# Kernel tuning notes

Hardware: AMD Instinct MI355X
Metric: run time of the kernel (lower is better)

## Reference

```python
import jax, jax.numpy as jnp
import numpy as np

H, FH, D = 8, 4, 64          # num_heads, focal_heads, att_size
HID = H * D                   # hidden_size = 512
B, S = 8, 512                 # batch, num_nodes
T_HOP, T_EDGE = 32, 16
SCALE = D ** -0.5


def setup_inputs() -> dict:
    key = jax.random.key(0)
    ks = jax.random.split(key, 24)
    f = lambda i, shape: jax.random.normal(ks[i], shape, jnp.float32)
    w = 1.0 / np.sqrt(HID)
    inp = {
        'q': f(0, (B, S, HID)), 'k': f(1, (B, S, HID)), 'v': f(2, (B, S, HID)),
        'query_hop_emb': f(3, (T_HOP, HID)) * 0.02,
        'query_edge_emb': f(4, (T_EDGE, HID)) * 0.02,
        'key_hop_emb': f(5, (T_HOP, HID)) * 0.02,
        'key_edge_emb': f(6, (T_EDGE, HID)) * 0.02,
        'value_hop_emb': f(7, (T_HOP, HID)) * 0.02,
        'value_edge_emb': f(8, (T_EDGE, HID)) * 0.02,
        'distance': jax.random.randint(ks[9], (B, S, S), 0, T_HOP),
        'edge_attr': jax.random.randint(ks[10], (B, S, S), 0, T_EDGE),
        # guarantee at least one unmasked key per query row to keep softmax finite
        'mask': jax.random.bernoulli(ks[11], 0.9, (B, S)).at[:, 0].set(True),
        'focal_mask': jax.random.bernoulli(ks[12], 0.5, (B, S, S)).at[:, :, 0].set(True),
        'Wq': f(13, (HID, H * D)) * w, 'bq': f(14, (H * D,)) * 0.01,
        'Wk': f(15, (HID, H * D)) * w, 'bk': f(16, (H * D,)) * 0.01,
        'Wv': f(17, (HID, H * D)) * w, 'bv': f(18, (H * D,)) * 0.01,
        'Wo': f(19, (H * D, HID)) * w, 'bo': f(20, (HID,)) * 0.01,
    }
    return inp


def _emb_scores(x, emb):
    # x: [B,H,S,D], emb: [T, H*D] -> per-head scores [B,H,S,T]
    e = emb.reshape(-1, H, D).transpose(1, 0, 2)  # [H,T,D]
    return jnp.einsum('bhsd,htd->bhst', x, e)


def _gather_last(scores, idx):
    # scores: [B,H,S,T], idx: [B,S,S] -> [B,H,S,S]
    idx_b = jnp.broadcast_to(idx[:, None], (B, H, S, S))
    return jnp.take_along_axis(scores, idx_b, axis=3)


def _scatter_add_last(attn, idx, T):
    # attn: [B,H,S,S], idx: [B,S,S] -> [B,H,S,T] accumulating attn weights
    idx_b = jnp.broadcast_to(idx[:, None], (B, H, S, S)).reshape(B * H * S, S)
    rows = jnp.arange(B * H * S)[:, None]
    flat = (rows * T + idx_b).reshape(-1)
    out = jnp.zeros((B * H * S * T,), attn.dtype).at[flat].add(attn.reshape(-1))
    return out.reshape(B, H, S, T)


def reference(q, k, v, query_hop_emb, query_edge_emb, key_hop_emb, key_edge_emb,
              value_hop_emb, value_edge_emb, distance, edge_attr, mask, focal_mask,
              Wq, bq, Wk, bk, Wv, bv, Wo, bo):
    qh = (q @ Wq + bq).reshape(B, S, H, D).transpose(0, 2, 1, 3)  # [B,H,S,D]
    kh = (k @ Wk + bk).reshape(B, S, H, D).transpose(0, 2, 1, 3)
    vh = (v @ Wv + bv).reshape(B, S, H, D).transpose(0, 2, 1, 3)

    spatial_bias = (_gather_last(_emb_scores(qh, query_hop_emb), distance)
                    + _gather_last(_emb_scores(kh, key_hop_emb), distance))
    edge_bias = (_gather_last(_emb_scores(qh, query_edge_emb), edge_attr)
                 + _gather_last(_emb_scores(kh, key_edge_emb), edge_attr))

    attn = (jnp.einsum('bhsd,bhtd->bhst', qh, kh) + spatial_bias + edge_bias) * SCALE

    GS = H - FH
    a1 = jnp.where(mask[:, None, None, :], attn[:, :GS], -jnp.inf)
    a2 = jnp.where(focal_mask[:, None], attn[:, GS:], -jnp.inf)
    attn = jax.nn.softmax(jnp.concatenate([a1, a2], axis=1), axis=3)

    vha = _scatter_add_last(attn, distance, T_HOP)   # [B,H,S,T_HOP]
    vea = _scatter_add_last(attn, edge_attr, T_EDGE)  # [B,H,S,T_EDGE]
    vh_emb = value_hop_emb.reshape(T_HOP, H, D).transpose(1, 0, 2)   # [H,T,D]
    ve_emb = value_edge_emb.reshape(T_EDGE, H, D).transpose(1, 0, 2)

    x = (jnp.einsum('bhst,bhtd->bhsd', attn, vh)
         + jnp.einsum('bhst,htd->bhsd', vha, vh_emb)
         + jnp.einsum('bhst,htd->bhsd', vea, ve_emb))
    x = x.transpose(0, 2, 1, 3).reshape(B, S, H * D)
    return x @ Wo + bo
```

## Files before the change

### kernel.cpp

```cpp
#include <hip/hip_runtime.h>

constexpr int nB = 8, nS = 512, nH = 8, nD = 64, nHID = 512;
constexpr int THOP = 32, TEDGE = 16;
constexpr float SCALE = 0.125f;
constexpr float NEGINF = -30000.0f;

typedef __attribute__((ext_vector_type(8))) short bf16x8;
typedef __attribute__((ext_vector_type(4))) float f32x4;

#define MFMA16(A, B, C) __builtin_amdgcn_mfma_f32_16x16x32_bf16(A, B, C, 0, 0, 0)

__device__ __align__(16) unsigned short g_qhi[(size_t)nB * nH * nS * nD];
__device__ __align__(16) unsigned short g_qlo[(size_t)nB * nH * nS * nD];
__device__ __align__(16) unsigned short g_khi[(size_t)nB * nH * nS * nD];
__device__ __align__(16) unsigned short g_klo[(size_t)nB * nH * nS * nD];
__device__ __align__(16) unsigned short g_vhiT[(size_t)nB * nH * nD * nS];
__device__ __align__(16) unsigned short g_vloT[(size_t)nB * nH * nD * nS];
__device__ __align__(16) unsigned short g_embh[96 * 512];
__device__ __align__(16) unsigned short g_embl[96 * 512];
__device__ __align__(16) unsigned short g_inhi[(size_t)3 * 2097152];
__device__ __align__(16) unsigned short g_inlo[(size_t)3 * 2097152];
__device__ __align__(16) unsigned short g_wth[(size_t)4 * 262144];
__device__ __align__(16) unsigned short g_wtl[(size_t)4 * 262144];
__device__ __align__(16) unsigned short g_xhi[(size_t)nB * nS * nHID];
__device__ __align__(16) unsigned short g_xlo[(size_t)nB * nS * nHID];
__device__ int g_flags[32];

__device__ __forceinline__ float ldf(const void* p, int isf32, size_t i) {
  if (isf32) return ((const float*)p)[i];
  unsigned int w = (unsigned int)(((const unsigned short*)p)[i]) << 16;
  return __uint_as_float(w);
}
__device__ __forceinline__ float bf2f(unsigned short h) {
  return __uint_as_float((unsigned)h << 16);
}
__device__ __forceinline__ float4 ldf4(const void* p, int isf32, size_t i) {
  if (isf32) return ((const float4*)p)[i >> 2];
  const ushort4 u = ((const ushort4*)p)[i >> 2];
  float4 r;
  r.x = bf2f(u.x); r.y = bf2f(u.y); r.z = bf2f(u.z); r.w = bf2f(u.w);
  return r;
}
__device__ __forceinline__ unsigned short f2bf(float x) {
  unsigned u = __float_as_uint(x);
  u += 0x7FFFu + ((u >> 16) & 1u);
  return (unsigned short)(u >> 16);
}

__device__ int detect_bool_mode(const unsigned char* p) {
  if (p[0] == 0x80 && p[1] == 0x3F) return 2;
  if (p[0] == 0x00 && p[1] == 0x3C) return 4;
  if (p[0] == 0x00 && p[3] == 0x3F) return 3;
  for (int i = 0; i < 64; i += 4)
    if (p[i + 1] | p[i + 2] | p[i + 3]) return 1;
  return 0;
}
__device__ __forceinline__ bool bool_at(const unsigned char* p, int mode, size_t i) {
  switch (mode) {
    case 0: return ((const int*)p)[i] != 0;
    case 1: return p[i] != 0;
    case 3: return ((const float*)p)[i] != 0.f;
    default: return ((const unsigned short*)p)[i] != 0;
  }
}

__global__ __launch_bounds__(256) void detect_all(
    const void* q, const void* k, const void* v,
    const void* qhe, const void* qee, const void* khe, const void* kee,
    const void* vhe, const void* vee,
    const int* dist, const int* edge,
    const unsigned char* mraw, const unsigned char* fraw,
    const void* Wq, const void* bq, const void* Wk, const void* bk,
    const void* Wv, const void* bv, const void* Wo, const void* bo) {
  __shared__ float sred[256];
  __shared__ int nzs;
  const int tid = threadIdx.x;
  const int blk = blockIdx.x;

  if (blk < 17) {
    const void* arrs[17] = {q, k, v, qhe, qee, khe, kee, vhe, vee,
                            Wq, bq, Wk, bk, Wv, bv, Wo, bo};
    const int full[17] = {2097152, 2097152, 2097152, 8192, 8192, 8192, 8192,
                          8192, 8192, 262144, 512, 262144, 512, 262144, 512,
                          262144, 512};
    const int n = full[blk] < 16384 ? full[blk] : 16384;
    const unsigned short* u = (const unsigned short*)arrs[blk];
    float m = 0.f;
    for (int i = tid; i < n; i += 256) {
      float x = __uint_as_float((unsigned int)u[i] << 16);
      if (x != x) x = 1e20f;
      m = fmaxf(m, fabsf(x));
    }
    sred[tid] = m;
    __syncthreads();
    for (int s = 128; s > 0; s >>= 1) {
      if (tid < s) sred[tid] = fmaxf(sred[tid], sred[tid + s]);
      __syncthreads();
    }
    if (tid == 0) g_flags[4 + blk] = (sred[0] > 1e3f) ? 1 : 0;
  } else if (blk == 17 || blk == 18) {
    const int* p = (blk == 17) ? dist : edge;
    if (tid == 0) nzs = 0;
    __syncthreads();
    int a = 0;
    for (int i = tid; i < 4096; i += 256) a |= p[2 * i + 1];
    if (a) atomicOr(&nzs, 1);
    __syncthreads();
    if (tid == 0) g_flags[blk - 17] = (nzs == 0);
  } else {
    if (tid == 0) {
      g_flags[2] = detect_bool_mode(mraw);
      g_flags[3] = detect_bool_mode(fraw);
    }
  }
}

__global__ __launch_bounds__(256) void emb_prep(
    const void* qhe, const void* khe, const void* qee, const void* kee) {
  const int blk = blockIdx.x;
  const void* srcs[4] = {qhe, khe, qee, kee};
  const int flagIdx[4] = {7, 9, 8, 10};
  const int counts[4] = {32 * 512, 32 * 512, 16 * 512, 16 * 512};
  const int dsts[4] = {0, 32 * 512, 64 * 512, 80 * 512};
  const int f = g_flags[flagIdx[blk]];
  const void* src = srcs[blk];
  const int n = counts[blk], d0 = dsts[blk];
  for (int i = threadIdx.x; i < n; i += 256) {
    const float x = ldf(src, f, i);
    const unsigned short hi = f2bf(x);
    g_embh[d0 + i] = hi;
    g_embl[d0 + i] = f2bf(x - bf2f(hi));
  }
}

__global__ __launch_bounds__(256) void split_prep(
    const void* q, const void* k, const void* v) {
  const int t = blockIdx.y;
  const void* srcs[3] = {q, k, v};
  const int f = g_flags[4 + t];
  const size_t base = (size_t)t * 2097152;
  const size_t i = ((size_t)blockIdx.x * 256 + threadIdx.x) * 4;
  const float4 v4 = ldf4(srcs[t], f, i);
  ushort4 h4, l4;
  h4.x = f2bf(v4.x); l4.x = f2bf(v4.x - bf2f(h4.x));
  h4.y = f2bf(v4.y); l4.y = f2bf(v4.y - bf2f(h4.y));
  h4.z = f2bf(v4.z); l4.z = f2bf(v4.z - bf2f(h4.z));
  h4.w = f2bf(v4.w); l4.w = f2bf(v4.w - bf2f(h4.w));
  *(ushort4*)&g_inhi[base + i] = h4;
  *(ushort4*)&g_inlo[base + i] = l4;
}

__global__ __launch_bounds__(256) void wt_prep(
    const void* Wq, const void* Wk, const void* Wv, const void* Wo) {
  __shared__ float t[64][65];
  const int mat = blockIdx.y;
  const void* srcs[4] = {Wq, Wk, Wv, Wo};
  const int fIdx[4] = {13, 15, 17, 19};
  const int f = g_flags[fIdx[mat]];
  const void* W = srcs[mat];
  const int k0 = (blockIdx.x >> 3) * 64, n0 = (blockIdx.x & 7) * 64;
  const int tid = threadIdx.x;
  const int r = tid >> 4, c4 = (tid & 15) * 4;
#pragma unroll
  for (int i = 0; i < 4; ++i) {
    const float4 v4 = ldf4(W, f, (size_t)(k0 + r + i * 16) * 512 + n0 + c4);
    t[r + i * 16][c4] = v4.x;
    t[r + i * 16][c4 + 1] = v4.y;
    t[r + i * 16][c4 + 2] = v4.z;
    t[r + i * 16][c4 + 3] = v4.w;
  }
  __syncthreads();
  unsigned short* dh = g_wth + (size_t)mat * 262144;
  unsigned short* dl = g_wtl + (size_t)mat * 262144;
#pragma unroll
  for (int i = 0; i < 4; ++i) {
    const int rn = r + i * 16;
    ushort4 h4, l4;
    const float v0 = t[c4][rn], v1 = t[c4 + 1][rn];
    const float v2 = t[c4 + 2][rn], v3 = t[c4 + 3][rn];
    h4.x = f2bf(v0); l4.x = f2bf(v0 - bf2f(h4.x));
    h4.y = f2bf(v1); l4.y = f2bf(v1 - bf2f(h4.y));
    h4.z = f2bf(v2); l4.z = f2bf(v2 - bf2f(h4.z));
    h4.w = f2bf(v3); l4.w = f2bf(v3 - bf2f(h4.w));
    *(ushort4*)&dh[(size_t)(n0 + rn) * 512 + k0 + c4] = h4;
    *(ushort4*)&dl[(size_t)(n0 + rn) * 512 + k0 + c4] = l4;
  }
}

__global__ __launch_bounds__(256) void gemm_mfma(
    const unsigned short* __restrict__ Ahi, const unsigned short* __restrict__ Alo,
    const unsigned short* __restrict__ Wth, const unsigned short* __restrict__ Wtl,
    const void* __restrict__ bias, int bFlag,
    float* __restrict__ dst, int mode) {
  __shared__ unsigned short As_hi[64][40];
  __shared__ unsigned short As_lo[64][40];
  __shared__ unsigned short Wt_hi[64][40];
  __shared__ unsigned short Wt_lo[64][40];
  const int bF = g_flags[bFlag];
  const int tid = threadIdx.x;
  const int m0 = blockIdx.y * 64, n0 = blockIdx.x * 64;
  const int w = tid >> 6, l = tid & 63, c = l & 15, g = l >> 4;
  const int wr = w >> 1, wc = w & 1;
  const int sr = tid >> 2, sc = (tid & 3) * 8;

  f32x4 acc[2][2] = {{{0.f, 0.f, 0.f, 0.f}, {0.f, 0.f, 0.f, 0.f}},
                     {{0.f, 0.f, 0.f, 0.f}, {0.f, 0.f, 0.f, 0.f}}};

  for (int k0 = 0; k0 < 512; k0 += 32) {
    __syncthreads();
    {
      const size_t ga = (size_t)(m0 + sr) * 512 + k0 + sc;
      const size_t gw = (size_t)(n0 + sr) * 512 + k0 + sc;
      const bf16x8 ah = *(const bf16x8*)(Ahi + ga);
      const bf16x8 al = *(const bf16x8*)(Alo + ga);
      const bf16x8 wh = *(const bf16x8*)(Wth + gw);
      const bf16x8 wl = *(const bf16x8*)(Wtl + gw);
      *(bf16x8*)&As_hi[sr][sc] = ah;
      *(bf16x8*)&As_lo[sr][sc] = al;
      *(bf16x8*)&Wt_hi[sr][sc] = wh;
      *(bf16x8*)&Wt_lo[sr][sc] = wl;
    }
    __syncthreads();
#pragma unroll
    for (int mi = 0; mi < 2; ++mi) {
      const bf16x8 ah = *(const bf16x8*)&As_hi[wr * 32 + mi * 16 + c][g * 8];
      const bf16x8 al = *(const bf16x8*)&As_lo[wr * 32 + mi * 16 + c][g * 8];
#pragma unroll
      for (int nj = 0; nj < 2; ++nj) {
        const bf16x8 wh = *(const bf16x8*)&Wt_hi[wc * 32 + nj * 16 + c][g * 8];
        const bf16x8 wl = *(const bf16x8*)&Wt_lo[wc * 32 + nj * 16 + c][g * 8];
        acc[mi][nj] = MFMA16(ah, wh, acc[mi][nj]);
        acc[mi][nj] = MFMA16(al, wh, acc[mi][nj]);
        acc[mi][nj] = MFMA16(ah, wl, acc[mi][nj]);
      }
    }
  }
#pragma unroll
  for (int mi = 0; mi < 2; ++mi)
#pragma unroll
    for (int nj = 0; nj < 2; ++nj)
#pragma unroll
      for (int r = 0; r < 4; ++r) {
        const int m = m0 + wr * 32 + mi * 16 + 4 * g + r;
        const int n = n0 + wc * 32 + nj * 16 + c;
        const float v2 = acc[mi][nj][r] + ldf(bias, bF, n);
        if (mode == 3) {
          dst[(size_t)m * 512 + n] = v2;
        } else {
          const int b = m >> 9, s = m & 511, h = n >> 6, d = n & 63;
          const unsigned short hi = f2bf(v2);
          const unsigned short lo = f2bf(v2 - bf2f(hi));
          if (mode == 0) {
            const size_t i0 = (((size_t)(b * nH + h) * nS) + s) * nD + d;
            g_qhi[i0] = hi; g_qlo[i0] = lo;
          } else if (mode == 1) {
            const size_t i0 = (((size_t)(b * nH + h) * nS) + s) * nD + d;
            g_khi[i0] = hi; g_klo[i0] = lo;
          } else {
            const size_t i0 = (((size_t)(b * nH + h) * nD) + d) * nS + s;
            g_vhiT[i0] = hi; g_vloT[i0] = lo;
          }
        }
      }
}

__global__ __launch_bounds__(256) void attn_kernel(
    const int* __restrict__ dist, const int* __restrict__ edge,
    const unsigned char* __restrict__ mraw, const unsigned char* __restrict__ fraw,
    const void* __restrict__ vhe, const void* __restrict__ vee) {
  __shared__ float chop_s[16][33];
  __shared__ float cedge_s[16][17];
  __shared__ float vha_s[16][33];
  __shared__ float vea_s[16][17];
  __shared__ float red_s[16][4];
  __shared__ float red2_s[16][4];
  __shared__ float rinv_s[16];
  __shared__ float x_s[64][17];
  __shared__ unsigned char dlds[16][516];
  __shared__ unsigned char elds[16][516];
  __shared__ unsigned char flds[16][516];
  __shared__ unsigned char smask_l[516];

  const int bh = blockIdx.x, qt = blockIdx.y;
  const int b = bh >> 3, h = bh & 7;
  const int q0 = qt * 16;
  const int tid = threadIdx.x;
  const int w = tid >> 6, l = tid & 63, c = l & 15, g = l >> 4;

  const int d64 = g_flags[0], e64 = g_flags[1];
  const int mmode = g_flags[2], fmode = g_flags[3];
  const int fvhe = g_flags[11], fvee = g_flags[12];

  for (int i = tid; i < 16 * 33; i += 256) (&vha_s[0][0])[i] = 0.f;
  for (int i = tid; i < 16 * 17; i += 256) (&vea_s[0][0])[i] = 0.f;
  for (int i = tid; i < 64 * 17; i += 256) (&x_s[0][0])[i] = 0.f;

  const size_t rowbase = ((size_t)b * nS + q0) * nS;
  if (!d64) {
    const int4* dp = (const int4*)(dist + rowbase);
    for (int j4 = tid; j4 < 2048; j4 += 256) {
      const int4 t = dp[j4];
      const int j = j4 * 4, r = j >> 9, c1 = j & 511;
      *(unsigned*)&dlds[r][c1] =
          (unsigned)(t.x & 31) | ((unsigned)(t.y & 31) << 8) |
          ((unsigned)(t.z & 31) << 16) | ((unsigned)(t.w & 31) << 24);
    }
  } else {
    const int4* dp = (const int4*)(dist + 2 * rowbase);
    for (int j2 = tid; j2 < 4096; j2 += 256) {
      const int4 t = dp[j2];
      const int j = j2 * 2, r = j >> 9, c1 = j & 511;
      *(unsigned short*)&dlds[r][c1] =
          (unsigned short)((t.x & 31) | ((t.z & 31) << 8));
    }
  }
  if (!e64) {
    const int4* ep = (const int4*)(edge + rowbase);
    for (int j4 = tid; j4 < 2048; j4 += 256) {
      const int4 t = ep[j4];
      const int j = j4 * 4, r = j >> 9, c1 = j & 511;
      *(unsigned*)&elds[r][c1] =
          (unsigned)(t.x & 15) | ((unsigned)(t.y & 15) << 8) |
          ((unsigned)(t.z & 15) << 16) | ((unsigned)(t.w & 15) << 24);
    }
  } else {
    const int4* ep = (const int4*)(edge + 2 * rowbase);
    for (int j2 = tid; j2 < 4096; j2 += 256) {
      const int4 t = ep[j2];
      const int j = j2 * 2, r = j >> 9, c1 = j & 511;
      *(unsigned short*)&elds[r][c1] =
          (unsigned short)((t.x & 15) | ((t.z & 15) << 8));
    }
  }
  if (h < 4) {
    for (int i4 = tid; i4 < 128; i4 += 256) {
      unsigned wv = 0;
#pragma unroll
      for (int t = 0; t < 4; ++t)
        wv |= (unsigned)bool_at(mraw, mmode, (size_t)b * nS + i4 * 4 + t) << (8 * t);
      *(unsigned*)&smask_l[i4 * 4] = wv;
    }
  } else {
    for (int i4 = tid; i4 < 2048; i4 += 256) {
      const int j = i4 * 4, r = j >> 9, c1 = j & 511;
      unsigned wv = 0;
#pragma unroll
      for (int t = 0; t < 4; ++t)
        wv |= (unsigned)bool_at(fraw, fmode, rowbase + j + t) << (8 * t);
      *(unsigned*)&flds[r][c1] = wv;
    }
  }

  const size_t qbase = (((size_t)bh * nS) + q0 + c) * nD + g * 8;
  const bf16x8 qh0 = *(const bf16x8*)(g_qhi + qbase);
  const bf16x8 qh1 = *(const bf16x8*)(g_qhi + qbase + 32);
  const bf16x8 ql0 = *(const bf16x8*)(g_qlo + qbase);
  const bf16x8 ql1 = *(const bf16x8*)(g_qlo + qbase + 32);

  if (w < 3) {
    const bool isEdge = (w == 2);
    const int tb = (w == 1) ? 16 : 0;
    const size_t qe0 = (isEdge ? (size_t)64 * 512 : 0) + (size_t)(tb + c) * 512 + h * 64;
    const size_t ke0 = (isEdge ? (size_t)80 * 512 : (size_t)32 * 512) + (size_t)(tb + c) * 512 + h * 64;
    f32x4 acc = {0.f, 0.f, 0.f, 0.f};
#pragma unroll
    for (int dh = 0; dh < 2; ++dh) {
      const bf16x8 qhh = dh ? qh1 : qh0;
      const bf16x8 qll = dh ? ql1 : ql0;
      const bf16x8 khq = *(const bf16x8*)(g_khi + qbase + dh * 32);
      const bf16x8 klq = *(const bf16x8*)(g_klo + qbase + dh * 32);
      const bf16x8 eqh = *(const bf16x8*)(g_embh + qe0 + dh * 32 + g * 8);
      const bf16x8 eql = *(const bf16x8*)(g_embl + qe0 + dh * 32 + g * 8);
      const bf16x8 ekh = *(const bf16x8*)(g_embh + ke0 + dh * 32 + g * 8);
      const bf16x8 ekl = *(const bf16x8*)(g_embl + ke0 + dh * 32 + g * 8);
      acc = MFMA16(qhh, eqh, acc);
      acc = MFMA16(qll, eqh, acc);
      acc = MFMA16(qhh, eql, acc);
      acc = MFMA16(khq, ekh, acc);
      acc = MFMA16(klq, ekh, acc);
      acc = MFMA16(khq, ekl, acc);
    }
    if (!isEdge) {
#pragma unroll
      for (int r = 0; r < 4; ++r) chop_s[4 * g + r][tb + c] = acc[r];
    } else {
#pragma unroll
      for (int r = 0; r < 4; ++r) cedge_s[4 * g + r][c] = acc[r];
    }
  }
  __syncthreads();

  f32x4 pS[8];
  const int kbw = w * 128;
#pragma unroll
  for (int kt = 0; kt < 8; ++kt) {
    const int kb = kbw + kt * 16;
    const size_t kbase = (((size_t)bh * nS) + kb + c) * nD + g * 8;
    f32x4 acc = {0.f, 0.f, 0.f, 0.f};
    {
      const bf16x8 kh0 = *(const bf16x8*)(g_khi + kbase);
      const bf16x8 kl0 = *(const bf16x8*)(g_klo + kbase);
      acc = MFMA16(kh0, qh0, acc);
      acc = MFMA16(kl0, qh0, acc);
      acc = MFMA16(kh0, ql0, acc);
      const bf16x8 kh1 = *(const bf16x8*)(g_khi + kbase + 32);
      const bf16x8 kl1 = *(const bf16x8*)(g_klo + kbase + 32);
      acc = MFMA16(kh1, qh1, acc);
      acc = MFMA16(kl1, qh1, acc);
      acc = MFMA16(kh1, ql1, acc);
    }
    const int key0 = kb + 4 * g;
    const unsigned dw = *(const unsigned*)&dlds[c][key0];
    const unsigned ew = *(const unsigned*)&elds[c][key0];
    const unsigned fw = (h < 4) ? *(const unsigned*)&smask_l[key0]
                                : *(const unsigned*)&flds[c][key0];
#pragma unroll
    for (int r = 0; r < 4; ++r) {
      const int dv = (dw >> (8 * r)) & 255;
      const int ev = (ew >> (8 * r)) & 255;
      const float s = (acc[r] + chop_s[c][dv] + cedge_s[c][ev]) * SCALE;
      pS[kt][r] = ((fw >> (8 * r)) & 255) ? s : NEGINF;
    }
  }

  float mx = NEGINF;
#pragma unroll
  for (int kt = 0; kt < 8; ++kt)
#pragma unroll
    for (int r = 0; r < 4; ++r) mx = fmaxf(mx, pS[kt][r]);
  mx = fmaxf(mx, __shfl_xor(mx, 16));
  mx = fmaxf(mx, __shfl_xor(mx, 32));
  if (l < 16) red_s[c][w] = mx;
  __syncthreads();
  const float M = fmaxf(fmaxf(red_s[c][0], red_s[c][1]),
                        fmaxf(red_s[c][2], red_s[c][3]));
  float sum = 0.f;
#pragma unroll
  for (int kt = 0; kt < 8; ++kt) {
    const int key0 = kbw + kt * 16 + 4 * g;
    const unsigned dw = *(const unsigned*)&dlds[c][key0];
    const unsigned ew = *(const unsigned*)&elds[c][key0];
#pragma unroll
    for (int r = 0; r < 4; ++r) {
      const float pv = __expf(pS[kt][r] - M);
      pS[kt][r] = pv;
      sum += pv;
      atomicAdd(&vha_s[c][(dw >> (8 * r)) & 255], pv);
      atomicAdd(&vea_s[c][(ew >> (8 * r)) & 255], pv);
    }
  }
  sum += __shfl_xor(sum, 16);
  sum += __shfl_xor(sum, 32);
  if (l < 16) red2_s[c][w] = sum;
  int pk[8][2];
#pragma unroll
  for (int kt = 0; kt < 8; ++kt) {
    pk[kt][0] = ((int)f2bf(pS[kt][1]) << 16) | (int)f2bf(pS[kt][0]);
    pk[kt][1] = ((int)f2bf(pS[kt][3]) << 16) | (int)f2bf(pS[kt][2]);
  }
  __syncthreads();
  if (w == 0 && l < 16) {
    const float tot = red2_s[c][0] + red2_s[c][1] + red2_s[c][2] + red2_s[c][3];
    rinv_s[c] = 1.0f / tot;
  }

  f32x4 oacc[4] = {{0.f, 0.f, 0.f, 0.f}, {0.f, 0.f, 0.f, 0.f},
                   {0.f, 0.f, 0.f, 0.f}, {0.f, 0.f, 0.f, 0.f}};
  const int srcA = ((g & 1) * 2) * 16 + c;
  const int srcB = srcA + 16;
  const bool hi2 = (g >> 1) != 0;
#pragma unroll
  for (int ks = 0; ks < 4; ++ks) {
    const int t0d0 = __shfl(pk[2 * ks][0], srcA);
    const int t1d0 = __shfl(pk[2 * ks + 1][0], srcA);
    const int t0d1 = __shfl(pk[2 * ks][1], srcA);
    const int t1d1 = __shfl(pk[2 * ks + 1][1], srcA);
    const int t0d0b = __shfl(pk[2 * ks][0], srcB);
    const int t1d0b = __shfl(pk[2 * ks + 1][0], srcB);
    const int t0d1b = __shfl(pk[2 * ks][1], srcB);
    const int t1d1b = __shfl(pk[2 * ks + 1][1], srcB);
    union { int i[4]; bf16x8 v; } bu;
    bu.i[0] = hi2 ? t1d0 : t0d0;
    bu.i[1] = hi2 ? t1d1 : t0d1;
    bu.i[2] = hi2 ? t1d0b : t0d0b;
    bu.i[3] = hi2 ? t1d1b : t0d1b;
    const int kk = w * 128 + ks * 32;
#pragma unroll
    for (int t = 0; t < 4; ++t) {
      const size_t vbase = (((size_t)bh * nD) + t * 16 + c) * nS + kk + g * 8;
      const bf16x8 vh_ = *(const bf16x8*)(g_vhiT + vbase);
      const bf16x8 vl_ = *(const bf16x8*)(g_vloT + vbase);
      oacc[t] = MFMA16(vh_, bu.v, oacc[t]);
      oacc[t] = MFMA16(vl_, bu.v, oacc[t]);
    }
  }
#pragma unroll
  for (int t = 0; t < 4; ++t)
#pragma unroll
    for (int r = 0; r < 4; ++r)
      atomicAdd(&x_s[t * 16 + 4 * g + r][c], oacc[t][r]);
  __syncthreads();

  {
    const int d = tid & 63, qq = tid >> 6;
    float val[4];
#pragma unroll
    for (int j = 0; j < 4; ++j) val[j] = x_s[d][qq + 4 * j];
    for (int t = 0; t < THOP; ++t) {
      const float e = ldf(vhe, fvhe, (size_t)t * nHID + h * 64 + d);
#pragma unroll
      for (int j = 0; j < 4; ++j) val[j] += vha_s[qq + 4 * j][t] * e;
    }
    for (int t = 0; t < TEDGE; ++t) {
      const float e = ldf(vee, fvee, (size_t)t * nHID + h * 64 + d);
#pragma unroll
      for (int j = 0; j < 4; ++j) val[j] += vea_s[qq + 4 * j][t] * e;
    }
#pragma unroll
    for (int j = 0; j < 4; ++j) {
      const int q = qq + 4 * j;
      const float xv = val[j] * rinv_s[q];
      const unsigned short hi = f2bf(xv);
      const size_t i0 = ((size_t)b * nS + q0 + q) * nHID + h * 64 + d;
      g_xhi[i0] = hi;
      g_xlo[i0] = f2bf(xv - bf2f(hi));
    }
  }
}

extern "C" void kernel_launch(void* const* d_in, const int* in_sizes, int n_in,
                              void* d_out, int out_size, void* d_ws, size_t ws_size,
                              hipStream_t stream) {
  const void* q   = d_in[0];
  const void* k   = d_in[1];
  const void* v   = d_in[2];
  const void* qhe = d_in[3];
  const void* qee = d_in[4];
  const void* khe = d_in[5];
  const void* kee = d_in[6];
  const void* vhe = d_in[7];
  const void* vee = d_in[8];
  const int* dist = (const int*)d_in[9];
  const int* edge = (const int*)d_in[10];
  const unsigned char* mraw = (const unsigned char*)d_in[11];
  const unsigned char* fraw = (const unsigned char*)d_in[12];
  const void* Wq = d_in[13];
  const void* bq = d_in[14];
  const void* Wk = d_in[15];
  const void* bk = d_in[16];
  const void* Wv = d_in[17];
  const void* bv = d_in[18];
  const void* Wo = d_in[19];
  const void* bo = d_in[20];

  detect_all<<<20, 256, 0, stream>>>(q, k, v, qhe, qee, khe, kee, vhe, vee,
                                     dist, edge, mraw, fraw,
                                     Wq, bq, Wk, bk, Wv, bv, Wo, bo);
  emb_prep<<<4, 256, 0, stream>>>(qhe, khe, qee, kee);
  split_prep<<<dim3(2048, 3), 256, 0, stream>>>(q, k, v);
  wt_prep<<<dim3(64, 4), 256, 0, stream>>>(Wq, Wk, Wv, Wo);

  unsigned short* inhi; hipGetSymbolAddress((void**)&inhi, HIP_SYMBOL(g_inhi));
  unsigned short* inlo; hipGetSymbolAddress((void**)&inlo, HIP_SYMBOL(g_inlo));
  unsigned short* wth;  hipGetSymbolAddress((void**)&wth,  HIP_SYMBOL(g_wth));
  unsigned short* wtl;  hipGetSymbolAddress((void**)&wtl,  HIP_SYMBOL(g_wtl));
  unsigned short* xhi;  hipGetSymbolAddress((void**)&xhi,  HIP_SYMBOL(g_xhi));
  unsigned short* xlo;  hipGetSymbolAddress((void**)&xlo,  HIP_SYMBOL(g_xlo));

  gemm_mfma<<<dim3(8, 64), 256, 0, stream>>>(inhi, inlo, wth, wtl,
                                             bq, 14, nullptr, 0);
  gemm_mfma<<<dim3(8, 64), 256, 0, stream>>>(inhi + 2097152, inlo + 2097152,
                                             wth + 262144, wtl + 262144,
                                             bk, 16, nullptr, 1);
  gemm_mfma<<<dim3(8, 64), 256, 0, stream>>>(inhi + 2 * 2097152, inlo + 2 * 2097152,
                                             wth + 2 * 262144, wtl + 2 * 262144,
                                             bv, 18, nullptr, 2);
  attn_kernel<<<dim3(64, 32), 256, 0, stream>>>(dist, edge, mraw, fraw, vhe, vee);
  gemm_mfma<<<dim3(8, 64), 256, 0, stream>>>(xhi, xlo,
                                             wth + 3 * 262144, wtl + 3 * 262144,
                                             bo, 20, (float*)d_out, 3);
}
```

Before: 661.8 us.

## Stage K/V tiles in swizzled LDS, pack indices/masks, prefetch GEMM tiles, remap blocks

The projection GEMM now prefetches the next k-slice into registers while computing on the current LDS tile, a form of software pipelining. The attention kernel packs distance, edge and mask into one 16-bit word per key in shared memory. It stages K in 64-row chunks and V-hi in 128-column chunks into XOR-swizzled shared buffers, cooperatively loaded, instead of per-lane global loads. Blocks are remapped so consecutive block IDs span different batch-heads, and x_s reuses the packed-index buffer to cut LDS footprint. The cost is many extra __syncthreads in the key and value loops and larger LDS use, which may lower occupancy.

```diff
diff --git a/kernel.cpp b/kernel.cpp
--- a/kernel.cpp
+++ b/kernel.cpp
@@ -206,21 +206,26 @@
   f32x4 acc[2][2] = {{{0.f, 0.f, 0.f, 0.f}, {0.f, 0.f, 0.f, 0.f}},
                      {{0.f, 0.f, 0.f, 0.f}, {0.f, 0.f, 0.f, 0.f}}};
 
+  const size_t ga = (size_t)(m0 + sr) * 512 + sc;
+  const size_t gw = (size_t)(n0 + sr) * 512 + sc;
+  bf16x8 pa_h = *(const bf16x8*)(Ahi + ga);
+  bf16x8 pa_l = *(const bf16x8*)(Alo + ga);
+  bf16x8 pw_h = *(const bf16x8*)(Wth + gw);
+  bf16x8 pw_l = *(const bf16x8*)(Wtl + gw);
+
   for (int k0 = 0; k0 < 512; k0 += 32) {
     __syncthreads();
-    {
-      const size_t ga = (size_t)(m0 + sr) * 512 + k0 + sc;
-      const size_t gw = (size_t)(n0 + sr) * 512 + k0 + sc;
-      const bf16x8 ah = *(const bf16x8*)(Ahi + ga);
-      const bf16x8 al = *(const bf16x8*)(Alo + ga);
-      const bf16x8 wh = *(const bf16x8*)(Wth + gw);
-      const bf16x8 wl = *(const bf16x8*)(Wtl + gw);
-      *(bf16x8*)&As_hi[sr][sc] = ah;
-      *(bf16x8*)&As_lo[sr][sc] = al;
-      *(bf16x8*)&Wt_hi[sr][sc] = wh;
-      *(bf16x8*)&Wt_lo[sr][sc] = wl;
-    }
-    __syncthreads();
+    *(bf16x8*)&As_hi[sr][sc] = pa_h;
+    *(bf16x8*)&As_lo[sr][sc] = pa_l;
+    *(bf16x8*)&Wt_hi[sr][sc] = pw_h;
+    *(bf16x8*)&Wt_lo[sr][sc] = pw_l;
+    __syncthreads();
+    if (k0 < 480) {
+      pa_h = *(const bf16x8*)(Ahi + ga + k0 + 32);
+      pa_l = *(const bf16x8*)(Alo + ga + k0 + 32);
+      pw_h = *(const bf16x8*)(Wth + gw + k0 + 32);
+      pw_l = *(const bf16x8*)(Wtl + gw + k0 + 32);
+    }
 #pragma unroll
     for (int mi = 0; mi < 2; ++mi) {
       const bf16x8 ah = *(const bf16x8*)&As_hi[wr * 32 + mi * 16 + c][g * 8];
@@ -268,6 +273,8 @@
     const int* __restrict__ dist, const int* __restrict__ edge,
     const unsigned char* __restrict__ mraw, const unsigned char* __restrict__ fraw,
     const void* __restrict__ vhe, const void* __restrict__ vee) {
+  __shared__ unsigned short kvbuf[8192];
+  __shared__ unsigned short plds[16][520];
   __shared__ float chop_s[16][33];
   __shared__ float cedge_s[16][17];
   __shared__ float vha_s[16][33];
@@ -275,13 +282,10 @@
   __shared__ float red_s[16][4];
   __shared__ float red2_s[16][4];
   __shared__ float rinv_s[16];
-  __shared__ float x_s[64][17];
-  __shared__ unsigned char dlds[16][516];
-  __shared__ unsigned char elds[16][516];
-  __shared__ unsigned char flds[16][516];
-  __shared__ unsigned char smask_l[516];
-
-  const int bh = blockIdx.x, qt = blockIdx.y;
+
+  const int id = blockIdx.x;
+  const int bh = (id & 7) * 8 + ((id >> 3) & 7);
+  const int qt = id >> 6;
   const int b = bh >> 3, h = bh & 7;
   const int q0 = qt * 16;
   const int tid = threadIdx.x;
@@ -293,62 +297,36 @@
 
   for (int i = tid; i < 16 * 33; i += 256) (&vha_s[0][0])[i] = 0.f;
   for (int i = tid; i < 16 * 17; i += 256) (&vea_s[0][0])[i] = 0.f;
-  for (int i = tid; i < 64 * 17; i += 256) (&x_s[0][0])[i] = 0.f;
 
   const size_t rowbase = ((size_t)b * nS + q0) * nS;
-  if (!d64) {
-    const int4* dp = (const int4*)(dist + rowbase);
-    for (int j4 = tid; j4 < 2048; j4 += 256) {
-      const int4 t = dp[j4];
-      const int j = j4 * 4, r = j >> 9, c1 = j & 511;
-      *(unsigned*)&dlds[r][c1] =
-          (unsigned)(t.x & 31) | ((unsigned)(t.y & 31) << 8) |
-          ((unsigned)(t.z & 31) << 16) | ((unsigned)(t.w & 31) << 24);
-    }
-  } else {
-    const int4* dp = (const int4*)(dist + 2 * rowbase);
-    for (int j2 = tid; j2 < 4096; j2 += 256) {
-      const int4 t = dp[j2];
-      const int j = j2 * 2, r = j >> 9, c1 = j & 511;
-      *(unsigned short*)&dlds[r][c1] =
-          (unsigned short)((t.x & 31) | ((t.z & 31) << 8));
-    }
-  }
-  if (!e64) {
-    const int4* ep = (const int4*)(edge + rowbase);
-    for (int j4 = tid; j4 < 2048; j4 += 256) {
-      const int4 t = ep[j4];
-      const int j = j4 * 4, r = j >> 9, c1 = j & 511;
-      *(unsigned*)&elds[r][c1] =
-          (unsigned)(t.x & 15) | ((unsigned)(t.y & 15) << 8) |
-          ((unsigned)(t.z & 15) << 16) | ((unsigned)(t.w & 15) << 24);
-    }
-  } else {
-    const int4* ep = (const int4*)(edge + 2 * rowbase);
-    for (int j2 = tid; j2 < 4096; j2 += 256) {
-      const int4 t = ep[j2];
-      const int j = j2 * 2, r = j >> 9, c1 = j & 511;
-      *(unsigned short*)&elds[r][c1] =
-          (unsigned short)((t.x & 15) | ((t.z & 15) << 8));
-    }
-  }
-  if (h < 4) {
-    for (int i4 = tid; i4 < 128; i4 += 256) {
-      unsigned wv = 0;
-#pragma unroll
-      for (int t = 0; t < 4; ++t)
-        wv |= (unsigned)bool_at(mraw, mmode, (size_t)b * nS + i4 * 4 + t) << (8 * t);
-      *(unsigned*)&smask_l[i4 * 4] = wv;
-    }
-  } else {
-    for (int i4 = tid; i4 < 2048; i4 += 256) {
-      const int j = i4 * 4, r = j >> 9, c1 = j & 511;
-      unsigned wv = 0;
-#pragma unroll
-      for (int t = 0; t < 4; ++t)
-        wv |= (unsigned)bool_at(fraw, fmode, rowbase + j + t) << (8 * t);
-      *(unsigned*)&flds[r][c1] = wv;
-    }
+  for (int j4 = tid; j4 < 2048; j4 += 256) {
+    const int j = j4 * 4, r = j >> 9, c1 = j & 511;
+    int dv[4], ev[4];
+    if (!d64) {
+      const int4 t = ((const int4*)(dist + rowbase))[j4];
+      dv[0] = t.x & 31; dv[1] = t.y & 31; dv[2] = t.z & 31; dv[3] = t.w & 31;
+    } else {
+      const int4 t0 = ((const int4*)(dist + 2 * rowbase))[2 * j4];
+      const int4 t1 = ((const int4*)(dist + 2 * rowbase))[2 * j4 + 1];
+      dv[0] = t0.x & 31; dv[1] = t0.z & 31; dv[2] = t1.x & 31; dv[3] = t1.z & 31;
+    }
+    if (!e64) {
+      const int4 t = ((const int4*)(edge + rowbase))[j4];
+      ev[0] = t.x & 15; ev[1] = t.y & 15; ev[2] = t.z & 15; ev[3] = t.w & 15;
+    } else {
+      const int4 t0 = ((const int4*)(edge + 2 * rowbase))[2 * j4];
+      const int4 t1 = ((const int4*)(edge + 2 * rowbase))[2 * j4 + 1];
+      ev[0] = t0.x & 15; ev[1] = t0.z & 15; ev[2] = t1.x & 15; ev[3] = t1.z & 15;
+    }
+    ushort4 pw;
+    unsigned short* pp = (unsigned short*)&pw;
+#pragma unroll
+    for (int t = 0; t < 4; ++t) {
+      const bool keep = (h < 4) ? bool_at(mraw, mmode, (size_t)b * nS + c1 + t)
+                                : bool_at(fraw, fmode, rowbase + j + t);
+      pp[t] = (unsigned short)(dv[t] | (ev[t] << 5) | ((int)keep << 9));
+    }
+    *(ushort4*)&plds[r][c1] = pw;
   }
 
   const size_t qbase = (((size_t)bh * nS) + q0 + c) * nD + g * 8;
@@ -388,38 +366,59 @@
       for (int r = 0; r < 4; ++r) cedge_s[4 * g + r][c] = acc[r];
     }
   }
+
+#pragma unroll
+  for (int it = 0; it < 2; ++it) {
+    const int e = (tid << 3) + (it << 11);
+    const int r = e >> 6, d0 = e & 63;
+    const size_t src = (((size_t)bh * nS) + r) * nD + d0;
+    const int dsti = (r << 6) + ((((d0 >> 3) ^ (r & 7))) << 3);
+    *(bf16x8*)&kvbuf[dsti] = *(const bf16x8*)(g_khi + src);
+    *(bf16x8*)&kvbuf[4096 + dsti] = *(const bf16x8*)(g_klo + src);
+  }
   __syncthreads();
 
   f32x4 pS[8];
-  const int kbw = w * 128;
-#pragma unroll
-  for (int kt = 0; kt < 8; ++kt) {
-    const int kb = kbw + kt * 16;
-    const size_t kbase = (((size_t)bh * nS) + kb + c) * nD + g * 8;
+  const int sw8 = c & 7;
+  for (int ch = 0; ch < 8; ++ch) {
+    const int rloc = w * 16 + c;
+    const int a0 = rloc << 6;
     f32x4 acc = {0.f, 0.f, 0.f, 0.f};
     {
-      const bf16x8 kh0 = *(const bf16x8*)(g_khi + kbase);
-      const bf16x8 kl0 = *(const bf16x8*)(g_klo + kbase);
+      const int o0 = a0 + ((g ^ sw8) << 3);
+      const int o1 = a0 + ((((4 + g) ^ sw8)) << 3);
+      const bf16x8 kh0 = *(const bf16x8*)&kvbuf[o0];
+      const bf16x8 kl0 = *(const bf16x8*)&kvbuf[4096 + o0];
+      const bf16x8 kh1 = *(const bf16x8*)&kvbuf[o1];
+      const bf16x8 kl1 = *(const bf16x8*)&kvbuf[4096 + o1];
       acc = MFMA16(kh0, qh0, acc);
       acc = MFMA16(kl0, qh0, acc);
       acc = MFMA16(kh0, ql0, acc);
-      const bf16x8 kh1 = *(const bf16x8*)(g_khi + kbase + 32);
-      const bf16x8 kl1 = *(const bf16x8*)(g_klo + kbase + 32);
       acc = MFMA16(kh1, qh1, acc);
       acc = MFMA16(kl1, qh1, acc);
       acc = MFMA16(kh1, ql1, acc);
     }
-    const int key0 = kb + 4 * g;
-    const unsigned dw = *(const unsigned*)&dlds[c][key0];
-    const unsigned ew = *(const unsigned*)&elds[c][key0];
-    const unsigned fw = (h < 4) ? *(const unsigned*)&smask_l[key0]
-                                : *(const unsigned*)&flds[c][key0];
+    const int key0 = ch * 64 + w * 16 + 4 * g;
+    const ushort4 pv4 = *(const ushort4*)&plds[c][key0];
+    const unsigned short pp[4] = {pv4.x, pv4.y, pv4.z, pv4.w};
 #pragma unroll
     for (int r = 0; r < 4; ++r) {
-      const int dv = (dw >> (8 * r)) & 255;
-      const int ev = (ew >> (8 * r)) & 255;
-      const float s = (acc[r] + chop_s[c][dv] + cedge_s[c][ev]) * SCALE;
-      pS[kt][r] = ((fw >> (8 * r)) & 255) ? s : NEGINF;
+      const float s = (acc[r] + chop_s[c][pp[r] & 31] +
+                       cedge_s[c][(pp[r] >> 5) & 15]) * SCALE;
+      pS[ch][r] = (pp[r] & 512) ? s : NEGINF;
+    }
+    __syncthreads();
+    if (ch < 7) {
+#pragma unroll
+      for (int it = 0; it < 2; ++it) {
+        const int e = (tid << 3) + (it << 11);
+        const int r = e >> 6, d0 = e & 63;
+        const size_t src = (((size_t)bh * nS) + (ch + 1) * 64 + r) * nD + d0;
+        const int dsti = (r << 6) + ((((d0 >> 3) ^ (r & 7))) << 3);
+        *(bf16x8*)&kvbuf[dsti] = *(const bf16x8*)(g_khi + src);
+        *(bf16x8*)&kvbuf[4096 + dsti] = *(const bf16x8*)(g_klo + src);
+      }
+      __syncthreads();
     }
   }
 
@@ -437,16 +436,16 @@
   float sum = 0.f;
 #pragma unroll
   for (int kt = 0; kt < 8; ++kt) {
-    const int key0 = kbw + kt * 16 + 4 * g;
-    const unsigned dw = *(const unsigned*)&dlds[c][key0];
-    const unsigned ew = *(const unsigned*)&elds[c][key0];
+    const int key0 = kt * 64 + w * 16 + 4 * g;
+    const ushort4 pv4 = *(const ushort4*)&plds[c][key0];
+    const unsigned short pp[4] = {pv4.x, pv4.y, pv4.z, pv4.w};
 #pragma unroll
     for (int r = 0; r < 4; ++r) {
       const float pv = __expf(pS[kt][r] - M);
       pS[kt][r] = pv;
       sum += pv;
-      atomicAdd(&vha_s[c][(dw >> (8 * r)) & 255], pv);
-      atomicAdd(&vea_s[c][(ew >> (8 * r)) & 255], pv);
+      atomicAdd(&vha_s[c][pp[r] & 31], pv);
+      atomicAdd(&vea_s[c][(pp[r] >> 5) & 15], pv);
     }
   }
   sum += __shfl_xor(sum, 16);
@@ -459,40 +458,53 @@
     pk[kt][1] = ((int)f2bf(pS[kt][3]) << 16) | (int)f2bf(pS[kt][2]);
   }
   __syncthreads();
+  float (*x_s)[17] = reinterpret_cast<float(*)[17]>(&plds[0][0]);
+  for (int i = tid; i < 64 * 17; i += 256) (&x_s[0][0])[i] = 0.f;
   if (w == 0 && l < 16) {
     const float tot = red2_s[c][0] + red2_s[c][1] + red2_s[c][2] + red2_s[c][3];
     rinv_s[c] = 1.0f / tot;
   }
+  __syncthreads();
 
   f32x4 oacc[4] = {{0.f, 0.f, 0.f, 0.f}, {0.f, 0.f, 0.f, 0.f},
                    {0.f, 0.f, 0.f, 0.f}, {0.f, 0.f, 0.f, 0.f}};
   const int srcA = ((g & 1) * 2) * 16 + c;
   const int srcB = srcA + 16;
   const bool hi2 = (g >> 1) != 0;
-#pragma unroll
-  for (int ks = 0; ks < 4; ++ks) {
-    const int t0d0 = __shfl(pk[2 * ks][0], srcA);
-    const int t1d0 = __shfl(pk[2 * ks + 1][0], srcA);
-    const int t0d1 = __shfl(pk[2 * ks][1], srcA);
-    const int t1d1 = __shfl(pk[2 * ks + 1][1], srcA);
-    const int t0d0b = __shfl(pk[2 * ks][0], srcB);
-    const int t1d0b = __shfl(pk[2 * ks + 1][0], srcB);
-    const int t0d1b = __shfl(pk[2 * ks][1], srcB);
-    const int t1d1b = __shfl(pk[2 * ks + 1][1], srcB);
+  for (int p = 0; p < 4; ++p) {
+#pragma unroll
+    for (int it = 0; it < 4; ++it) {
+      const int e = (tid << 3) + (it << 11);
+      const int d = e >> 7, colc = e & 127;
+      const size_t src = (((size_t)bh * nD) + d) * nS + (p << 7) + colc;
+      const int dsti = (d << 7) + ((((colc >> 3) ^ (d & 15))) << 3);
+      *(bf16x8*)&kvbuf[dsti] = *(const bf16x8*)(g_vhiT + src);
+    }
+    __syncthreads();
+    const int t0d0 = __shfl(pk[2 * p][0], srcA);
+    const int t1d0 = __shfl(pk[2 * p + 1][0], srcA);
+    const int t0d1 = __shfl(pk[2 * p][1], srcA);
+    const int t1d1 = __shfl(pk[2 * p + 1][1], srcA);
+    const int t0d0b = __shfl(pk[2 * p][0], srcB);
+    const int t1d0b = __shfl(pk[2 * p + 1][0], srcB);
+    const int t0d1b = __shfl(pk[2 * p][1], srcB);
+    const int t1d1b = __shfl(pk[2 * p + 1][1], srcB);
     union { int i[4]; bf16x8 v; } bu;
     bu.i[0] = hi2 ? t1d0 : t0d0;
     bu.i[1] = hi2 ? t1d1 : t0d1;
     bu.i[2] = hi2 ? t1d0b : t0d0b;
     bu.i[3] = hi2 ? t1d1b : t0d1b;
-    const int kk = w * 128 + ks * 32;
+    const int col16 = (w << 1) + (g & 1) + ((g >> 1) << 3);
+    const int j0 = (p << 7) + ((g >> 1) << 6) + (w << 4) + ((g & 1) << 3);
 #pragma unroll
     for (int t = 0; t < 4; ++t) {
-      const size_t vbase = (((size_t)bh * nD) + t * 16 + c) * nS + kk + g * 8;
-      const bf16x8 vh_ = *(const bf16x8*)(g_vhiT + vbase);
-      const bf16x8 vl_ = *(const bf16x8*)(g_vloT + vbase);
+      const int row = t * 16 + c;
+      const bf16x8 vh_ = *(const bf16x8*)&kvbuf[(row << 7) + (((col16 ^ c)) << 3)];
+      const bf16x8 vl_ = *(const bf16x8*)(g_vloT + (((size_t)bh * nD) + row) * nS + j0);
       oacc[t] = MFMA16(vh_, bu.v, oacc[t]);
       oacc[t] = MFMA16(vl_, bu.v, oacc[t]);
     }
+    __syncthreads();
   }
 #pragma unroll
   for (int t = 0; t < 4; ++t)
@@ -575,7 +587,7 @@
   gemm_mfma<<<dim3(8, 64), 256, 0, stream>>>(inhi + 2 * 2097152, inlo + 2 * 2097152,
                                              wth + 2 * 262144, wtl + 2 * 262144,
                                              bv, 18, nullptr, 2);
-  attn_kernel<<<dim3(64, 32), 256, 0, stream>>>(dist, edge, mraw, fraw, vhe, vee);
+  attn_kernel<<<2048, 256, 0, stream>>>(dist, edge, mraw, fraw, vhe, vee);
   gemm_mfma<<<dim3(8, 64), 256, 0, stream>>>(xhi, xlo,
                                              wth + 3 * 262144, wtl + 3 * 262144,
                                              bo, 20, (float*)d_out, 3);
```

After: 649.1 us. About the same (-1.9%).
